# Optimization experiments

Hardware: AMD Instinct MI355X
Metric: run time of the kernel (lower is better)

The kernel has to match this reference:

```python
import jax, jax.numpy as jnp
import numpy as np

ATOM_FDIM = 133
BOND_FDIM = 147
HIDDEN = 300
DEPTH = 3
N_ATOMS = 100000
N_BONDS = 200000
MAX_NB = 6
N_MOLS = 4000


def setup_inputs() -> dict:
    key = jax.random.key(0)
    ks = jax.random.split(key, 10)
    f_atoms = jax.random.normal(ks[0], (N_ATOMS, ATOM_FDIM), dtype=jnp.float32)
    f_bonds = jax.random.normal(ks[1], (N_BONDS, BOND_FDIM), dtype=jnp.float32)
    a2b = jax.random.randint(ks[2], (N_ATOMS, MAX_NB), 0, N_BONDS)
    b2a = jax.random.randint(ks[3], (N_BONDS,), 0, N_ATOMS)
    b2revb = jax.random.randint(ks[4], (N_BONDS,), 0, N_BONDS)
    atom2mol = jnp.sort(jax.random.randint(ks[5], (N_ATOMS,), 0, N_MOLS))
    s = 1.0 / np.sqrt(HIDDEN)
    W_i = jax.random.uniform(ks[6], (BOND_FDIM, HIDDEN), jnp.float32, -s, s)
    W_h = jax.random.uniform(ks[7], (HIDDEN, HIDDEN), jnp.float32, -s, s)
    W_o_w = jax.random.uniform(ks[8], (ATOM_FDIM + HIDDEN, HIDDEN), jnp.float32, -s, s)
    W_o_b = jax.random.uniform(ks[9], (HIDDEN,), jnp.float32, -s, s)
    return {"f_atoms": f_atoms, "f_bonds": f_bonds, "a2b": a2b, "b2a": b2a,
            "b2revb": b2revb, "atom2mol": atom2mol, "W_i": W_i, "W_h": W_h,
            "W_o_w": W_o_w, "W_o_b": W_o_b}


def reference(f_atoms, f_bonds, a2b, b2a, b2revb, atom2mol, W_i, W_h, W_o_w, W_o_b):
    # input = W_i(f_bonds); message = act(input)
    inp = f_bonds @ W_i                      # [n_bonds, hidden]
    message = jax.nn.relu(inp)
    for _ in range(DEPTH - 1):
        # gather neighbor bond messages per atom and sum: [n_atoms, max_nb, h] -> [n_atoms, h]
        a_message = message[a2b].sum(axis=1)
        rev_message = message[b2revb]        # [n_bonds, hidden]
        message = a_message[b2a] - rev_message
        message = jax.nn.relu(inp + message @ W_h)
    # final atom-level aggregation
    a_message = message[a2b].sum(axis=1)     # [n_atoms, hidden]
    a_input = jnp.concatenate([f_atoms, a_message], axis=1)
    atom_hiddens = jax.nn.relu(a_input @ W_o_w + W_o_b)
    # segment mean pooling over molecules
    sums = jax.ops.segment_sum(atom_hiddens, atom2mol, num_segments=N_MOLS)
    counts = jax.ops.segment_sum(jnp.ones((atom_hiddens.shape[0],), atom_hiddens.dtype),
                                 atom2mol, num_segments=N_MOLS)
    mol_vecs = sums / jnp.maximum(counts, 1.0)[:, None]  # zero vec for empty mols
    return mol_vecs
```

## Files before the change

kernel.cpp:

```cpp
#include <hip/hip_runtime.h>
#include <stdint.h>

#define ATOM_FDIM 133
#define BOND_FDIM 147
#define HIDDEN    300
#define N_ATOMS   100000
#define N_BONDS   200000
#define MAX_NB    6
#define N_MOLS    4000

#define KP_I 192
#define KP_H 320
#define KP_O 512
#define LDA  304
#define CPR  38

#define TM   128
#define BCH  20

typedef unsigned short u16;
typedef short bf16x8 __attribute__((ext_vector_type(8)));
typedef float f32x4 __attribute__((ext_vector_type(4)));

__device__ __forceinline__ u16 f2bu(float f) {
    unsigned u = __float_as_uint(f);
    u += 0x7FFFu + ((u >> 16) & 1u);
    return (u16)(u >> 16);
}
__device__ __forceinline__ float bu2f(u16 b) { return __uint_as_float(((unsigned)b) << 16); }

__device__ __forceinline__ uint4 relu_bf16x8(uint4 v) {
    union { uint4 u; u16 s[8]; } x, o;
    x.u = v;
    #pragma unroll
    for (int e = 0; e < 8; ++e) o.s[e] = (x.s[e] & 0x8000u) ? (u16)0 : x.s[e];
    return o.u;
}
__device__ __forceinline__ uint4 comb_bf16x8(uint4 vi, uint4 va, uint4 vy) {
    union { uint4 u; u16 s[8]; } xi, xa, xy, o;
    xi.u = vi; xa.u = va; xy.u = vy;
    #pragma unroll
    for (int e = 0; e < 8; ++e)
        o.s[e] = f2bu(fmaxf(bu2f(xi.s[e]) + bu2f(xa.s[e]) - bu2f(xy.s[e]), 0.f));
    return o.u;
}

#define AS1 __attribute__((address_space(1)))
#define AS3 __attribute__((address_space(3)))
__device__ __forceinline__ void gl_lds(const void* g, void* l) {
    __builtin_amdgcn_global_load_lds((const AS1 void*)g, (AS3 void*)l, 16, 0, 0);
}
#define MFMA(a, b, c) __builtin_amdgcn_mfma_f32_16x16x32_bf16((a), (b), (c), 0, 0, 0)

template <int EPI>
__global__ __launch_bounds__(512, 2) void mm_k(
    const u16* __restrict__ A, int lda,
    const u16* __restrict__ Wp,
    const float* __restrict__ bias,
    u16* __restrict__ out0, int ldo0,
    int M, int NT)
{
    __shared__ __align__(16) u16 As[3][16 * 512];
    __shared__ __align__(16) u16 Bs[2][40 * 512];

    const int t    = threadIdx.x;
    const int lane = t & 63, wid = t >> 6;
    const int fl   = lane & 15, fh = lane >> 4;
    const int m0   = blockIdx.x * TM;
    const int wr   = wid >> 1, wc = wid & 1;

    int arow = m0 + wid * 16 + fl;
    if (arow > M - 1) arow = M - 1;
    const char* srcAp = (const char*)A + (size_t)arow * (size_t)lda * 2u + (size_t)(fh * 16);
    const char* WpC = (const char*)Wp;
    const size_t srcB0 = (size_t)(5 * wid) * 1024u + (size_t)lane * 16u;

    f32x4 acc[2][10] = {};

#define STAGE_A(kt, buf) do {                                                      \
        gl_lds(srcAp + (size_t)(kt) * 128u,      (char*)As[buf] + wid * 1024);     \
        gl_lds(srcAp + (size_t)(kt) * 128u + 64, (char*)As[buf] + 8192 + wid * 1024); \
    } while (0)
#define STAGE_B(kt, buf) do {                                                      \
        const size_t kb_ = (size_t)(kt) * 40960u;                                  \
        _Pragma("unroll")                                                          \
        for (int j = 0; j < 5; ++j)                                                \
            gl_lds(WpC + kb_ + srcB0 + (size_t)j * 1024,                           \
                   (char*)Bs[buf] + 5 * wid * 1024 + j * 1024);                    \
    } while (0)

    STAGE_A(0, 0);
    STAGE_B(0, 0);
    STAGE_A(1, 1);
    asm volatile("s_waitcnt vmcnt(2)" ::: "memory");
    __builtin_amdgcn_s_barrier();

    int cur = 0;
    for (int tt = 0; tt < NT; ++tt) {
        int w1 = tt + 1; if (w1 >= NT) w1 -= NT;
        int w2 = tt + 2; if (w2 >= NT) w2 -= NT;
        const int nx1 = (cur < 2) ? cur + 1 : 0;
        const int nx2 = (nx1 < 2) ? nx1 + 1 : 0;
        const u16* as_c = As[cur];
        const u16* bs_c = Bs[tt & 1];

        bf16x8 af0, af1, bfv[10];
        af0 = *reinterpret_cast<const bf16x8*>(&as_c[(wr * 2 + 0) * 512 + lane * 8]);
        af1 = *reinterpret_cast<const bf16x8*>(&as_c[(wr * 2 + 1) * 512 + lane * 8]);
        #pragma unroll
        for (int n = 0; n < 10; ++n)
            bfv[n] = *reinterpret_cast<const bf16x8*>(&bs_c[(wc * 10 + n) * 512 + lane * 8]);
        STAGE_B(w1, (tt + 1) & 1);
        __builtin_amdgcn_s_barrier();
        __builtin_amdgcn_s_setprio(1);
        #pragma unroll
        for (int n = 0; n < 10; ++n) {
            acc[0][n] = MFMA(af0, bfv[n], acc[0][n]);
            acc[1][n] = MFMA(af1, bfv[n], acc[1][n]);
        }
        __builtin_amdgcn_s_setprio(0);
        __builtin_amdgcn_s_barrier();

        af0 = *reinterpret_cast<const bf16x8*>(&as_c[(8 + wr * 2 + 0) * 512 + lane * 8]);
        af1 = *reinterpret_cast<const bf16x8*>(&as_c[(8 + wr * 2 + 1) * 512 + lane * 8]);
        #pragma unroll
        for (int n = 0; n < 10; ++n)
            bfv[n] = *reinterpret_cast<const bf16x8*>(&bs_c[(20 + wc * 10 + n) * 512 + lane * 8]);
        STAGE_A(w2, nx2);
        asm volatile("s_waitcnt vmcnt(2)" ::: "memory");
        __builtin_amdgcn_s_barrier();
        __builtin_amdgcn_s_setprio(1);
        #pragma unroll
        for (int n = 0; n < 10; ++n) {
            acc[0][n] = MFMA(af0, bfv[n], acc[0][n]);
            acc[1][n] = MFMA(af1, bfv[n], acc[1][n]);
        }
        __builtin_amdgcn_s_setprio(0);
        __builtin_amdgcn_s_barrier();
        cur = nx1;
    }
#undef STAGE_A
#undef STAGE_B

    #pragma unroll
    for (int m = 0; m < 2; ++m) {
        #pragma unroll
        for (int r = 0; r < 4; ++r) {
            const int row = m0 + wr * 32 + m * 16 + fh * 4 + r;
            if (row >= M) continue;
            #pragma unroll
            for (int n = 0; n < 10; ++n) {
                const int col = wc * 160 + n * 16 + fl;
                if (col >= HIDDEN) continue;
                const float v = acc[m][n][r];
                if (EPI == 1) out0[(size_t)row * ldo0 + col] = f2bu(v);
                else          out0[(size_t)row * ldo0 + col] = f2bu(fmaxf(v + bias[col], 0.f));
            }
        }
    }
}

template <int AM>
__global__ __launch_bounds__(512, 2) void mmf_k(
    const u16* __restrict__ A, int lda,
    const u16* __restrict__ aYp,
    const u16* __restrict__ Yp,
    const int* __restrict__ b2a,
    const int* __restrict__ b2revb,
    const u16* __restrict__ Wp,
    u16* __restrict__ out0, int ldo0,
    int M, int NT)
{
    __shared__ __align__(16) u16 As[2][16 * 512];
    __shared__ __align__(16) u16 Bs[2][40 * 512];

    const int t    = threadIdx.x;
    const int lane = t & 63, wid = t >> 6;
    const int fl   = lane & 15, fh = lane >> 4;
    const int m0   = blockIdx.x * TM;
    const int wr   = wid >> 1, wc = wid & 1;

    int arow = m0 + wid * 16 + fl;
    if (arow > M - 1) arow = M - 1;
    const char* pI = (const char*)A + (size_t)arow * (size_t)lda * 2u + (size_t)(fh * 16);
    const char* pA = nullptr; const char* pY = nullptr;
    if constexpr (AM == 2) {
        const int ia = b2a[arow], ir = b2revb[arow];
        pA = (const char*)aYp + (size_t)ia * (LDA * 2) + (size_t)(fh * 16);
        pY = (const char*)Yp  + (size_t)ir * (LDA * 2) + (size_t)(fh * 16);
    }
    const char* WpC = (const char*)Wp;
    const size_t srcB0 = (size_t)(5 * wid) * 1024u + (size_t)lane * 16u;

    f32x4 acc[2][10] = {};
    uint4 Xi0, Xi1, Xa0, Xa1, Xy0, Xy1;
    uint4 Yi0, Yi1, Ya0, Ya1, Yy0, Yy1;
    (void)Xa0; (void)Xa1; (void)Xy0; (void)Xy1;
    (void)Ya0; (void)Ya1; (void)Yy0; (void)Yy1;

#define STAGE_B(kt, buf) do {                                                      \
        const size_t kb_ = (size_t)(kt) * 40960u;                                  \
        _Pragma("unroll")                                                          \
        for (int j = 0; j < 5; ++j)                                                \
            gl_lds(WpC + kb_ + srcB0 + (size_t)j * 1024,                           \
                   (char*)Bs[buf] + 5 * wid * 1024 + j * 1024);                    \
    } while (0)
#define LOADSET(kt, I0, I1, A0, A1, Y0, Y1) do {                                   \
        const size_t kb_ = (size_t)(kt) * 128u;                                    \
        I0 = *reinterpret_cast<const uint4*>(pI + kb_);                            \
        I1 = *reinterpret_cast<const uint4*>(pI + kb_ + 64);                       \
        if constexpr (AM == 2) {                                                   \
            A0 = *reinterpret_cast<const uint4*>(pA + kb_);                        \
            A1 = *reinterpret_cast<const uint4*>(pA + kb_ + 64);                   \
            Y0 = *reinterpret_cast<const uint4*>(pY + kb_);                        \
            Y1 = *reinterpret_cast<const uint4*>(pY + kb_ + 64);                   \
        }                                                                          \
    } while (0)
#define XF(I, Aa, Yy) (AM == 2 ? comb_bf16x8(I, Aa, Yy) : relu_bf16x8(I))

    LOADSET(0, Xi0, Xi1, Xa0, Xa1, Xy0, Xy1);
    STAGE_B(0, 0);
    LOADSET(1, Yi0, Yi1, Ya0, Ya1, Yy0, Yy1);
    if constexpr (AM == 2) asm volatile("s_waitcnt vmcnt(11)" ::: "memory");
    else                   asm volatile("s_waitcnt vmcnt(7)"  ::: "memory");
    *reinterpret_cast<uint4*>(&As[0][wid * 512 + lane * 8])       = XF(Xi0, Xa0, Xy0);
    *reinterpret_cast<uint4*>(&As[0][(8 + wid) * 512 + lane * 8]) = XF(Xi1, Xa1, Xy1);
    if constexpr (AM == 2) asm volatile("s_waitcnt vmcnt(6)" ::: "memory");
    else                   asm volatile("s_waitcnt vmcnt(2)" ::: "memory");
    asm volatile("s_waitcnt lgkmcnt(0)" ::: "memory");
    __builtin_amdgcn_s_barrier();

    int tt = 0;

#define STEP(LI0, LI1, LA0, LA1, LY0, LY1, WI0, WI1, WA0, WA1, WY0, WY1) do {               \
    int w1 = tt + 1; if (w1 >= NT) w1 -= NT;                                                \
    int w2 = tt + 2; if (w2 >= NT) w2 -= NT;                                                \
    const u16* as_c = As[tt & 1];                                                           \
    const u16* bs_c = Bs[tt & 1];                                                           \
    bf16x8 af0, af1, bfv[10];                                                               \
                                                                     \
    af0 = *reinterpret_cast<const bf16x8*>(&as_c[(wr * 2 + 0) * 512 + lane * 8]);           \
    af1 = *reinterpret_cast<const bf16x8*>(&as_c[(wr * 2 + 1) * 512 + lane * 8]);           \
    _Pragma("unroll")                                                                       \
    for (int n = 0; n < 10; ++n)                                                            \
        bfv[n] = *reinterpret_cast<const bf16x8*>(&bs_c[(wc * 10 + n) * 512 + lane * 8]);   \
    STAGE_B(w1, (tt + 1) & 1);                                        \
    LOADSET(w2, LI0, LI1, LA0, LA1, LY0, LY1);                                              \
    __builtin_amdgcn_s_barrier();                                                           \
    __builtin_amdgcn_s_setprio(1);                                                          \
    _Pragma("unroll")                                                                       \
    for (int n = 0; n < 10; ++n) {                                                          \
        acc[0][n] = MFMA(af0, bfv[n], acc[0][n]);                                           \
        acc[1][n] = MFMA(af1, bfv[n], acc[1][n]);                                           \
    }                                                                                       \
    __builtin_amdgcn_s_setprio(0);                                                          \
    __builtin_amdgcn_s_barrier();                                                           \
                                                                     \
    af0 = *reinterpret_cast<const bf16x8*>(&as_c[(8 + wr * 2 + 0) * 512 + lane * 8]);       \
    af1 = *reinterpret_cast<const bf16x8*>(&as_c[(8 + wr * 2 + 1) * 512 + lane * 8]);       \
    _Pragma("unroll")                                                                       \
    for (int n = 0; n < 10; ++n)                                                            \
        bfv[n] = *reinterpret_cast<const bf16x8*>(&bs_c[(20 + wc * 10 + n) * 512 + lane * 8]); \
    if constexpr (AM == 2) asm volatile("s_waitcnt vmcnt(6)" ::: "memory");                 \
    else                   asm volatile("s_waitcnt vmcnt(2)" ::: "memory");                 \
    *reinterpret_cast<uint4*>(&As[(tt + 1) & 1][wid * 512 + lane * 8])       = XF(WI0, WA0, WY0); \
    *reinterpret_cast<uint4*>(&As[(tt + 1) & 1][(8 + wid) * 512 + lane * 8]) = XF(WI1, WA1, WY1); \
    asm volatile("s_waitcnt lgkmcnt(0)" ::: "memory");                                      \
    __builtin_amdgcn_s_barrier();                                                           \
    __builtin_amdgcn_s_setprio(1);                                                          \
    _Pragma("unroll")                                                                       \
    for (int n = 0; n < 10; ++n) {                                                          \
        acc[0][n] = MFMA(af0, bfv[n], acc[0][n]);                                           \
        acc[1][n] = MFMA(af1, bfv[n], acc[1][n]);                                           \
    }                                                                                       \
    __builtin_amdgcn_s_setprio(0);                                                          \
    __builtin_amdgcn_s_barrier();                                                           \
    ++tt;                                                                                   \
} while (0)

    while (tt + 1 < NT) {
        STEP(Xi0, Xi1, Xa0, Xa1, Xy0, Xy1, Yi0, Yi1, Ya0, Ya1, Yy0, Yy1);
        STEP(Yi0, Yi1, Ya0, Ya1, Yy0, Yy1, Xi0, Xi1, Xa0, Xa1, Xy0, Xy1);
    }
    if (tt < NT) STEP(Xi0, Xi1, Xa0, Xa1, Xy0, Xy1, Yi0, Yi1, Ya0, Ya1, Yy0, Yy1);
#undef STEP
#undef LOADSET
#undef STAGE_B
#undef XF

    #pragma unroll
    for (int m = 0; m < 2; ++m) {
        #pragma unroll
        for (int r = 0; r < 4; ++r) {
            const int row = m0 + wr * 32 + m * 16 + fh * 4 + r;
            if (row >= M) continue;
            #pragma unroll
            for (int n = 0; n < 10; ++n) {
                const int col = wc * 160 + n * 16 + fl;
                if (col >= HIDDEN) continue;
                out0[(size_t)row * ldo0 + col] = f2bu(acc[m][n][r]);
            }
        }
    }
}

__global__ __launch_bounds__(256) void wconv_k(const float* __restrict__ W,
                                               int split, int off1, int Ktot, int NT32,
                                               u16* __restrict__ Wp)
{
    const int id = blockIdx.x * 256 + threadIdx.x;
    if (id >= NT32 * BCH * 512) return;
    const int block = id >> 9, rem = id & 511;
    const int l = rem >> 3, e = rem & 7;
    const int c = block % BCH, kt = block / BCH;
    const int col = c * 16 + (l & 15);
    const int k   = kt * 32 + (l >> 4) * 8 + e;
    float v = 0.f;
    if (col < HIDDEN) {
        if (k < split) {
            const int r = k + off1;
            if (r < Ktot) v = W[(size_t)r * HIDDEN + col];
        } else {
            const int r = k - split;
            if (r < off1) v = W[(size_t)r * HIDDEN + col];
        }
    }
    Wp[id] = f2bu(v);
}

__global__ __launch_bounds__(256) void fbconv_k(const float* __restrict__ fb, u16* __restrict__ dst)
{
    const int id = blockIdx.x * 256 + threadIdx.x;
    if (id >= N_BONDS * KP_I) return;
    const int r = id / KP_I, k = id - r * KP_I;
    dst[id] = f2bu(k < BOND_FDIM ? fb[(size_t)r * BOND_FDIM + k] : 0.f);
}

__global__ __launch_bounds__(256) void agg_k(const u16* __restrict__ src,
                                             const int* __restrict__ a2b,
                                             u16* __restrict__ dst)
{
    const int c = blockIdx.x * 256 + threadIdx.x;
    if (c >= N_ATOMS * CPR) return;
    const int a = c / CPR, q = c - a * CPR;
    const int h = q * 8;
    const int* nb = a2b + (size_t)a * MAX_NB;
    float s[8] = {};
    #pragma unroll
    for (int j = 0; j < MAX_NB; ++j) {
        const int r = nb[j];
        union { uint4 u; u16 s[8]; } x;
        x.u = *(const uint4*)(src + (size_t)r * LDA + h);
        #pragma unroll
        for (int e = 0; e < 8; ++e) s[e] += bu2f(x.s[e]);
    }
    union { uint4 u; u16 s[8]; } o;
    #pragma unroll
    for (int e = 0; e < 8; ++e) o.s[e] = f2bu(s[e]);
    *(uint4*)(dst + (size_t)a * LDA + h) = o.u;
}

__global__ __launch_bounds__(256) void comb_k(const u16* __restrict__ inp,
                                              const u16* __restrict__ aY,
                                              const u16* __restrict__ Y,
                                              const int* __restrict__ b2a,
                                              const int* __restrict__ b2revb,
                                              u16* __restrict__ msg)
{
    const int c = blockIdx.x * 256 + threadIdx.x;
    if (c >= N_BONDS * CPR) return;
    const int b = c / CPR, q = c - b * CPR;
    const int h = q * 8;
    const int ia = b2a[b], ir = b2revb[b];
    union { uint4 u; u16 s[8]; } xi, xa, xy, o;
    xi.u = *(const uint4*)(inp + (size_t)b * LDA + h);
    xa.u = *(const uint4*)(aY + (size_t)ia * LDA + h);
    xy.u = *(const uint4*)(Y + (size_t)ir * LDA + h);
    #pragma unroll
    for (int j = 0; j < 8; ++j)
        o.s[j] = f2bu(fmaxf(bu2f(xi.s[j]) + bu2f(xa.s[j]) - bu2f(xy.s[j]), 0.f));
    *(uint4*)(msg + (size_t)b * LDA + h) = o.u;
}

__global__ __launch_bounds__(256) void aggcat_k(const u16* __restrict__ msg,
                                                const int* __restrict__ a2b,
                                                const float* __restrict__ fa,
                                                u16* __restrict__ dst)
{
    const int id = blockIdx.x * 256 + threadIdx.x;
    if (id >= N_ATOMS * (KP_O / 4)) return;
    const int a = id / (KP_O / 4), c = id - a * (KP_O / 4);
    const int e0 = c * 4;
    union { uint2 u; u16 s[4]; } o;
    if (e0 < HIDDEN) {
        const int* nb = a2b + (size_t)a * MAX_NB;
        float s0 = 0.f, s1 = 0.f, s2 = 0.f, s3 = 0.f;
        #pragma unroll
        for (int j = 0; j < MAX_NB; ++j) {
            union { uint2 u; u16 s[4]; } x;
            x.u = *(const uint2*)(msg + (size_t)nb[j] * LDA + e0);
            s0 += bu2f(x.s[0]); s1 += bu2f(x.s[1]); s2 += bu2f(x.s[2]); s3 += bu2f(x.s[3]);
        }
        o.s[0] = f2bu(s0); o.s[1] = f2bu(s1); o.s[2] = f2bu(s2); o.s[3] = f2bu(s3);
    } else {
        #pragma unroll
        for (int j = 0; j < 4; ++j) {
            const int fi = e0 + j - HIDDEN;
            o.s[j] = (fi >= 0 && fi < ATOM_FDIM) ? f2bu(fa[(size_t)a * ATOM_FDIM + fi]) : (u16)0;
        }
    }
    *(uint2*)(dst + (size_t)a * KP_O + e0) = o.u;
}

__global__ __launch_bounds__(320) void pool_k(const u16* __restrict__ ah,
                                              const int* __restrict__ a2m,
                                              float* __restrict__ out)
{
    const int m = blockIdx.x;
    int lo, hi;
    { int l = 0, r = N_ATOMS;
      while (l < r) { int mid = (l + r) >> 1; if (a2m[mid] < m) l = mid + 1; else r = mid; }
      lo = l; }
    { int l = lo, r = N_ATOMS;
      while (l < r) { int mid = (l + r) >> 1; if (a2m[mid] < m + 1) l = mid + 1; else r = mid; }
      hi = l; }
    const float inv = 1.0f / (float)((hi - lo) > 1 ? (hi - lo) : 1);
    const int h = threadIdx.x;
    if (h >= HIDDEN) return;
    float s = 0.f;
    for (int a = lo; a < hi; ++a) s += bu2f(ah[(size_t)a * LDA + h]);
    out[(size_t)m * HIDDEN + h] = s * inv;
}

extern "C" void kernel_launch(void* const* d_in, const int* in_sizes, int n_in,
                              void* d_out, int out_size, void* d_ws, size_t ws_size,
                              hipStream_t stream)
{
    const float* f_atoms  = (const float*)d_in[0];
    const float* f_bonds  = (const float*)d_in[1];
    const int*   a2b      = (const int*)d_in[2];
    const int*   b2a      = (const int*)d_in[3];
    const int*   b2revb   = (const int*)d_in[4];
    const int*   atom2mol = (const int*)d_in[5];
    const float* W_i      = (const float*)d_in[6];
    const float* W_h      = (const float*)d_in[7];
    const float* W_o_w    = (const float*)d_in[8];
    const float* W_o_b    = (const float*)d_in[9];
    float* out = (float*)d_out;

    char* p = (char*)d_ws;
    auto alloc = [&](size_t bytes) { char* r = p; p += (bytes + 255) & ~(size_t)255; return r; };
    u16* B0 = (u16*)alloc(((size_t)N_BONDS + 16) * LDA * 2);
    u16* B1 = (u16*)alloc(((size_t)N_BONDS + 16) * LDA * 2);
    u16* B2 = (u16*)alloc(((size_t)N_BONDS + 16) * LDA * 2);
    u16* aY = (u16*)alloc(((size_t)N_ATOMS + 16) * LDA * 2);
    u16* Wpi = (u16*)alloc((size_t)(KP_I / 32) * BCH * 512 * 2);
    u16* Wph = (u16*)alloc((size_t)(KP_H / 32) * BCH * 512 * 2);
    u16* Wpo = (u16*)alloc((size_t)(KP_O / 32) * BCH * 512 * 2);
    if ((size_t)(p - (char*)d_ws) > ws_size) return;

    u16* inp    = B0;
    u16* fb16   = B1;
    u16* Y1     = B1;
    u16* Y2     = B2;
    u16* msg2   = B1;
    u16* concat = B2;
    u16* ah     = B0;

    const dim3 blk(256);
    auto g1 = [](long long n) { return dim3((unsigned)((n + 255) / 256)); };
    const dim3 blk5(512);
    const dim3 gB((N_BONDS + TM - 1) / TM);
    const dim3 gA((N_ATOMS + TM - 1) / TM);

    const int BIGSPLIT = 1 << 20;
    wconv_k<<<g1((long long)(KP_I / 32) * BCH * 512), blk, 0, stream>>>(
        W_i, BIGSPLIT, 0, BOND_FDIM, KP_I / 32, Wpi);
    wconv_k<<<g1((long long)(KP_H / 32) * BCH * 512), blk, 0, stream>>>(
        W_h, BIGSPLIT, 0, HIDDEN, KP_H / 32, Wph);
    wconv_k<<<g1((long long)(KP_O / 32) * BCH * 512), blk, 0, stream>>>(
        W_o_w, HIDDEN, ATOM_FDIM, ATOM_FDIM + HIDDEN, KP_O / 32, Wpo);
    fbconv_k<<<g1((long long)N_BONDS * KP_I), blk, 0, stream>>>(f_bonds, fb16);

    mm_k<1><<<gB, blk5, 0, stream>>>(fb16, KP_I, Wpi, nullptr,
                                     inp, LDA, N_BONDS, KP_I / 64);

    mmf_k<1><<<gB, blk5, 0, stream>>>(inp, LDA, nullptr, nullptr, nullptr, nullptr,
                                      Wph, Y1, LDA, N_BONDS, KP_H / 64);
    agg_k<<<g1((long long)N_ATOMS * CPR), blk, 0, stream>>>(Y1, a2b, aY);

    mmf_k<2><<<gB, blk5, 0, stream>>>(inp, LDA, aY, Y1, b2a, b2revb,
                                      Wph, Y2, LDA, N_BONDS, KP_H / 64);
    agg_k<<<g1((long long)N_ATOMS * CPR), blk, 0, stream>>>(Y2, a2b, aY);

    comb_k<<<g1((long long)N_BONDS * CPR), blk, 0, stream>>>(inp, aY, Y2, b2a, b2revb, msg2);
    aggcat_k<<<g1((long long)N_ATOMS * (KP_O / 4)), blk, 0, stream>>>(msg2, a2b, f_atoms, concat);

    mm_k<2><<<gA, blk5, 0, stream>>>(concat, KP_O, Wpo, W_o_b,
                                     ah, LDA, N_ATOMS, KP_O / 64);
    pool_k<<<dim3(N_MOLS), dim3(320), 0, stream>>>(ah, atom2mol, out);
}
```

Before: 849.3 us.

## Use 32-wide K steps in mm_k to cut zero-padding of K dims

The mm_k GEMM now steps through K in chunks of 32 instead of 64. This lets the padded K sizes drop from 192 to 160 for the W_i GEMM and from 512 to 448 for the output GEMM, which removes wasted MFMA work and memory traffic on zero padding. A and B tiles are now triple-buffered together, and B-tile loads are split unevenly across waves. Each half-iteration issues part of the next-next stage, with per-wave vmcnt gates. Iterations double and barriers per unit of K double, which adds synchronization overhead.

```diff
diff --git a/kernel.cpp b/kernel.cpp
--- a/kernel.cpp
+++ b/kernel.cpp
@@ -9,13 +9,14 @@
 #define MAX_NB    6
 #define N_MOLS    4000
 
-#define KP_I 192
+#define KP_I 160
 #define KP_H 320
-#define KP_O 512
+#define KP_O 448
 #define LDA  304
 #define CPR  38
 
 #define TM   128
+#define ACH  8
 #define BCH  20
 
 typedef unsigned short u16;
@@ -60,8 +61,8 @@
     u16* __restrict__ out0, int ldo0,
     int M, int NT)
 {
-    __shared__ __align__(16) u16 As[3][16 * 512];
-    __shared__ __align__(16) u16 Bs[2][40 * 512];
+    __shared__ __align__(16) u16 As[3][ACH * 512];
+    __shared__ __align__(16) u16 Bs[3][BCH * 512];
 
     const int t    = threadIdx.x;
     const int lane = t & 63, wid = t >> 6;
@@ -73,65 +74,68 @@
     if (arow > M - 1) arow = M - 1;
     const char* srcAp = (const char*)A + (size_t)arow * (size_t)lda * 2u + (size_t)(fh * 16);
     const char* WpC = (const char*)Wp;
-    const size_t srcB0 = (size_t)(5 * wid) * 1024u + (size_t)lane * 16u;
+    const int bbase = (wid < 4) ? 3 * wid : 12 + 2 * (wid - 4);
+    const size_t srcB0 = (size_t)bbase * 1024u + (size_t)lane * 16u;
 
     f32x4 acc[2][10] = {};
 
-#define STAGE_A(kt, buf) do {                                                      \
-        gl_lds(srcAp + (size_t)(kt) * 128u,      (char*)As[buf] + wid * 1024);     \
-        gl_lds(srcAp + (size_t)(kt) * 128u + 64, (char*)As[buf] + 8192 + wid * 1024); \
+#define STAGE_T(kt, buf) do {                                                    \
+        const size_t kbB_ = (size_t)(kt) * (size_t)(BCH * 1024);                 \
+        gl_lds(srcAp + (size_t)(kt) * 64u, (char*)As[buf] + wid * 1024);         \
+        gl_lds(WpC + kbB_ + srcB0,        (char*)Bs[buf] + bbase * 1024);        \
+        gl_lds(WpC + kbB_ + srcB0 + 1024, (char*)Bs[buf] + bbase * 1024 + 1024); \
+        if (wid < 4)                                                             \
+            gl_lds(WpC + kbB_ + srcB0 + 2048, (char*)Bs[buf] + bbase * 1024 + 2048); \
     } while (0)
-#define STAGE_B(kt, buf) do {                                                      \
-        const size_t kb_ = (size_t)(kt) * 40960u;                                  \
-        _Pragma("unroll")                                                          \
-        for (int j = 0; j < 5; ++j)                                                \
-            gl_lds(WpC + kb_ + srcB0 + (size_t)j * 1024,                           \
-                   (char*)Bs[buf] + 5 * wid * 1024 + j * 1024);                    \
+
+#define GATE() do {                                                        \
+        if (wid < 4) asm volatile("s_waitcnt vmcnt(4)" ::: "memory");      \
+        else         asm volatile("s_waitcnt vmcnt(3)" ::: "memory");      \
     } while (0)
 
-    STAGE_A(0, 0);
-    STAGE_B(0, 0);
-    STAGE_A(1, 1);
-    asm volatile("s_waitcnt vmcnt(2)" ::: "memory");
+    STAGE_T(0, 0);
+    STAGE_T(1, 1);
+    GATE();
     __builtin_amdgcn_s_barrier();
 
     int cur = 0;
     for (int tt = 0; tt < NT; ++tt) {
-        int w1 = tt + 1; if (w1 >= NT) w1 -= NT;
         int w2 = tt + 2; if (w2 >= NT) w2 -= NT;
         const int nx1 = (cur < 2) ? cur + 1 : 0;
         const int nx2 = (nx1 < 2) ? nx1 + 1 : 0;
         const u16* as_c = As[cur];
-        const u16* bs_c = Bs[tt & 1];
+        const u16* bs_c = Bs[cur];
+        const size_t kbB = (size_t)w2 * (size_t)(BCH * 1024);
 
         bf16x8 af0, af1, bfv[10];
         af0 = *reinterpret_cast<const bf16x8*>(&as_c[(wr * 2 + 0) * 512 + lane * 8]);
         af1 = *reinterpret_cast<const bf16x8*>(&as_c[(wr * 2 + 1) * 512 + lane * 8]);
         #pragma unroll
-        for (int n = 0; n < 10; ++n)
+        for (int n = 0; n < 5; ++n)
             bfv[n] = *reinterpret_cast<const bf16x8*>(&bs_c[(wc * 10 + n) * 512 + lane * 8]);
-        STAGE_B(w1, (tt + 1) & 1);
+        gl_lds(srcAp + (size_t)w2 * 64u, (char*)As[nx2] + wid * 1024);
+        gl_lds(WpC + kbB + srcB0, (char*)Bs[nx2] + bbase * 1024);
         __builtin_amdgcn_s_barrier();
         __builtin_amdgcn_s_setprio(1);
         #pragma unroll
-        for (int n = 0; n < 10; ++n) {
+        for (int n = 0; n < 5; ++n) {
             acc[0][n] = MFMA(af0, bfv[n], acc[0][n]);
             acc[1][n] = MFMA(af1, bfv[n], acc[1][n]);
         }
         __builtin_amdgcn_s_setprio(0);
         __builtin_amdgcn_s_barrier();
 
-        af0 = *reinterpret_cast<const bf16x8*>(&as_c[(8 + wr * 2 + 0) * 512 + lane * 8]);
-        af1 = *reinterpret_cast<const bf16x8*>(&as_c[(8 + wr * 2 + 1) * 512 + lane * 8]);
-        #pragma unroll
-        for (int n = 0; n < 10; ++n)
-            bfv[n] = *reinterpret_cast<const bf16x8*>(&bs_c[(20 + wc * 10 + n) * 512 + lane * 8]);
-        STAGE_A(w2, nx2);
-        asm volatile("s_waitcnt vmcnt(2)" ::: "memory");
+        #pragma unroll
+        for (int n = 5; n < 10; ++n)
+            bfv[n] = *reinterpret_cast<const bf16x8*>(&bs_c[(wc * 10 + n) * 512 + lane * 8]);
+        gl_lds(WpC + kbB + srcB0 + 1024, (char*)Bs[nx2] + bbase * 1024 + 1024);
+        if (wid < 4)
+            gl_lds(WpC + kbB + srcB0 + 2048, (char*)Bs[nx2] + bbase * 1024 + 2048);
+        GATE();
         __builtin_amdgcn_s_barrier();
         __builtin_amdgcn_s_setprio(1);
         #pragma unroll
-        for (int n = 0; n < 10; ++n) {
+        for (int n = 5; n < 10; ++n) {
             acc[0][n] = MFMA(af0, bfv[n], acc[0][n]);
             acc[1][n] = MFMA(af1, bfv[n], acc[1][n]);
         }
@@ -139,8 +143,8 @@
         __builtin_amdgcn_s_barrier();
         cur = nx1;
     }
-#undef STAGE_A
-#undef STAGE_B
+#undef STAGE_T
+#undef GATE
 
     #pragma unroll
     for (int m = 0; m < 2; ++m) {
@@ -483,7 +487,7 @@
     fbconv_k<<<g1((long long)N_BONDS * KP_I), blk, 0, stream>>>(f_bonds, fb16);
 
     mm_k<1><<<gB, blk5, 0, stream>>>(fb16, KP_I, Wpi, nullptr,
-                                     inp, LDA, N_BONDS, KP_I / 64);
+                                     inp, LDA, N_BONDS, KP_I / 32);
 
     mmf_k<1><<<gB, blk5, 0, stream>>>(inp, LDA, nullptr, nullptr, nullptr, nullptr,
                                       Wph, Y1, LDA, N_BONDS, KP_H / 64);
@@ -497,6 +501,6 @@
     aggcat_k<<<g1((long long)N_ATOMS * (KP_O / 4)), blk, 0, stream>>>(msg2, a2b, f_atoms, concat);
 
     mm_k<2><<<gA, blk5, 0, stream>>>(concat, KP_O, Wpo, W_o_b,
-                                     ah, LDA, N_ATOMS, KP_O / 64);
+                                     ah, LDA, N_ATOMS, KP_O / 32);
     pool_k<<<dim3(N_MOLS), dim3(320), 0, stream>>>(ah, atom2mol, out);
 }
```

After: 819.0 us. 3.6% less time.
